# Performance work log

Measured on AMD Instinct MI355X. Metric: run time of the kernel, lower is better.

The kernel has to match this reference:

```python
import jax, jax.numpy as jnp
import numpy as np

B = 4096        # batch_size
D = 256         # feature_dim
N = 9000000     # dataset size (state buffer length)
G = 100         # num_groups
ALPHA = 0.5     # alpha_weight
GAMMA = 0.8
RHO = 8.0
LAM = 1.0       # lambada
ETA_P = 0.01
EPS = 1e-14
CLIP = 5.0


def setup_inputs() -> dict:
    key = jax.random.key(0)
    k = jax.random.split(key, 6)
    zis = jax.random.normal(k[0], (B, D), jnp.float32)
    zjs = jax.random.normal(k[1], (B, D), jnp.float32)
    # per-sample learned temperatures, small positive values
    taus_I = 0.01 + 0.2 * jax.random.uniform(k[2], (N,), jnp.float32)
    taus_T = 0.01 + 0.2 * jax.random.uniform(k[3], (N,), jnp.float32)
    group_info_I = jax.random.randint(k[4], (N,), 0, G, dtype=jnp.int32)
    group_info_T = jax.random.randint(k[5], (N,), 0, G, dtype=jnp.int32)
    ids = jnp.arange(B, dtype=jnp.int32)  # unique sample indices
    zeros_N = jnp.zeros((N,), jnp.float32)
    return {
        "zis": zis, "zjs": zjs,
        "s_I": zeros_N, "s_T": zeros_N, "b_I": zeros_N, "b_T": zeros_N,
        "z_I": jnp.zeros((G,), jnp.float32), "z_T": jnp.zeros((G,), jnp.float32),
        "p_I": jnp.ones((G,), jnp.float32) / G, "p_T": jnp.ones((G,), jnp.float32) / G,
        "taus_I": taus_I, "taus_T": taus_T,
        "ids": ids, "group_info_I": group_info_I, "group_info_T": group_info_T,
    }


def _l2norm(x):
    return x / jnp.maximum(jnp.linalg.norm(x, axis=1, keepdims=True), 1e-12)


def reference(zis, zjs, s_I, s_T, b_I, b_T, z_I, z_T, p_I, p_T,
              taus_I, taus_T, ids, group_info_I, group_info_T):
    zis = _l2norm(zis)
    zjs = _l2norm(zjs)
    sim = zis @ zjs.T                                   # [B, B]
    diag = jnp.diagonal(sim)                            # [B]
    mask_neg = 1.0 - jnp.eye(B, dtype=sim.dtype)
    image_diffs = sim - diag[:, None]
    text_diffs = sim - diag[None, :]

    tau_I = taus_I[ids]                                 # [B]
    tau_T = taus_T[ids]
    idt = jax.lax.stop_gradient(image_diffs / tau_I[:, None])
    tdt = jax.lax.stop_gradient(text_diffs / tau_T[None, :])

    # running max state (numerically-stable exp)
    old_b_I = b_I[ids]
    b_I_new = jnp.maximum(jnp.max(idt, axis=1), old_b_I)    # [B]
    old_b_T = b_T[ids]
    b_T_new = jnp.maximum(jnp.max(tdt, axis=0), old_b_T)    # [B]
    b_I = b_I.at[ids].set(b_I_new)
    b_T = b_T.at[ids].set(b_T_new)

    exp_I = jnp.exp(idt - b_I_new[:, None]) * mask_neg
    exp_T = jnp.exp(tdt - b_T_new[None, :]) * mask_neg
    g_I = jnp.sum(exp_I, axis=1)                         # [B]
    g_T = jnp.sum(exp_T, axis=0)                         # [B]

    # EMA of softmax denominators with max-rescaling
    s_I_new = (1.0 - GAMMA) * s_I[ids] * jnp.exp(old_b_I - b_I_new) + GAMMA * g_I
    s_T_new = (1.0 - GAMMA) * s_T[ids] * jnp.exp(old_b_T - b_T_new) + GAMMA * g_T
    s_I = s_I.at[ids].set(s_I_new)
    s_T = s_T.at[ids].set(s_T_new)
    s_I_c = jnp.maximum(s_I_new, EPS)
    s_T_c = jnp.maximum(s_T_new, EPS)

    w_I = exp_I / s_I_c[:, None]
    w_T = exp_T / s_T_c[None, :]

    gid_I = group_info_I[ids]                            # [B]
    gid_T = group_info_T[ids]
    gw_I = G * p_I[gid_I]                                # [B]
    gw_T = G * p_T[gid_T]

    image_loss = jnp.sum(w_I * gw_I[:, None] * image_diffs, axis=1)   # [B]
    text_loss = jnp.sum(w_T * gw_T[None, :] * text_diffs, axis=0)     # [B]
    total_loss = ALPHA * image_loss.mean() + (1.0 - ALPHA) * text_loss.mean()

    # per-group adversarial weight update
    F_I = tau_I * (jnp.log(s_I_c) + b_I_new + RHO)       # [B]
    F_T = tau_T * (jnp.log(s_T_c) + b_T_new + RHO)
    ones_b = jnp.ones((B,), sim.dtype)
    cnt_I = jnp.maximum(jax.ops.segment_sum(ones_b, gid_I, num_segments=G), 1.0)
    cnt_T = jnp.maximum(jax.ops.segment_sum(ones_b, gid_T, num_segments=G), 1.0)
    grad_p_I = jax.ops.segment_sum(F_I, gid_I, num_segments=G) / cnt_I
    grad_p_T = jax.ops.segment_sum(F_T, gid_T, num_segments=G) / cnt_T

    z_I = (1.0 - GAMMA) * z_I + GAMMA * grad_p_I
    z_T = (1.0 - GAMMA) * z_T + GAMMA * grad_p_T
    grad_hp_I = -LAM * jnp.log(p_I + EPS) - LAM
    grad_hp_T = -LAM * jnp.log(p_T + EPS) - LAM
    new_p_I = p_I * jnp.exp(2.0 * ETA_P * jnp.clip(z_I + grad_hp_I, -CLIP, CLIP))
    new_p_T = p_T * jnp.exp(2.0 * ETA_P * jnp.clip(z_T + grad_hp_T, -CLIP, CLIP))
    p_I = new_p_I / new_p_I.sum()
    p_T = new_p_T / new_p_T.sum()

    return total_loss, p_I, p_T
```

## Files before the change

### kernel.cpp

```cpp
#include <hip/hip_runtime.h>
#include <hip/hip_bf16.h>
#include <math.h>

#define BB 4096
#define DD 256
#define GG 100
#define GAMMA_C 0.8f
#define RHO_C 8.0f
#define ALPHA_C 0.5f
#define EPS_C 1e-14f
#define NSR 64
#define NSC 32

typedef __bf16 bf16x8 __attribute__((ext_vector_type(8)));
typedef float f32x16 __attribute__((ext_vector_type(16)));

__device__ inline int swzLoc(int r31, int k) {
    return ((k >> 4) << 9) | (((((k >> 3) & 1) << 5) | r31) << 3) | (k & 7);
}

__device__ inline float blockReduceSum(float v, float* lds) {
    for (int o = 32; o > 0; o >>= 1) v += __shfl_down(v, o);
    int lane = threadIdx.x & 63, wid = threadIdx.x >> 6;
    if (lane == 0) lds[wid] = v;
    __syncthreads();
    if (threadIdx.x == 0) {
        float r = lds[0];
        int nw = blockDim.x >> 6;
        for (int w = 1; w < nw; w++) r += lds[w];
        lds[0] = r;
    }
    __syncthreads();
    float r = lds[0];
    __syncthreads();
    return r;
}

__global__ void __launch_bounds__(256) norm_kernel(const float* __restrict__ zis,
                            const float* __restrict__ zjs,
                            ushort* __restrict__ zhi, ushort* __restrict__ zlo,
                            ushort* __restrict__ whi, ushort* __restrict__ wlo,
                            float* __restrict__ diag, float* __restrict__ acc) {
    __shared__ ushort st[4][8192];
    int rb = blockIdx.x;
    int wv = threadIdx.x >> 6, lane = threadIdx.x & 63;
    if (rb == 0) { acc[threadIdx.x] = 0.f; acc[threadIdx.x + 256] = 0.f; }
    for (int rr = 0; rr < 8; rr++) {
        int r = rb * 32 + wv * 8 + rr;
        float4 zv = *(const float4*)&zis[r * DD + lane * 4];
        float4 wv4 = *(const float4*)&zjs[r * DD + lane * 4];
        float sz = zv.x * zv.x + zv.y * zv.y + zv.z * zv.z + zv.w * zv.w;
        float sw = wv4.x * wv4.x + wv4.y * wv4.y + wv4.z * wv4.z + wv4.w * wv4.w;
        float dt = zv.x * wv4.x + zv.y * wv4.y + zv.z * wv4.z + zv.w * wv4.w;
        for (int mask = 1; mask <= 32; mask <<= 1) {
            sz += __shfl_xor(sz, mask);
            sw += __shfl_xor(sw, mask);
            dt += __shfl_xor(dt, mask);
        }
        float iz = 1.0f / fmaxf(sqrtf(sz), 1e-12f);
        float iw = 1.0f / fmaxf(sqrtf(sw), 1e-12f);
        if (lane == 0) diag[r] = dt * iz * iw;
        float nz[4] = {zv.x * iz, zv.y * iz, zv.z * iz, zv.w * iz};
        float nw[4] = {wv4.x * iw, wv4.y * iw, wv4.z * iw, wv4.w * iw};
        int r31 = wv * 8 + rr;
        for (int e = 0; e < 4; e++) {
            int k = lane * 4 + e;
            int li = swzLoc(r31, k);
            __hip_bfloat16 hz = __float2bfloat16(nz[e]);
            __hip_bfloat16 lz = __float2bfloat16(nz[e] - __bfloat162float(hz));
            __hip_bfloat16 hw = __float2bfloat16(nw[e]);
            __hip_bfloat16 lw = __float2bfloat16(nw[e] - __bfloat162float(hw));
            st[0][li] = *(ushort*)&hz;
            st[1][li] = *(ushort*)&lz;
            st[2][li] = *(ushort*)&hw;
            st[3][li] = *(ushort*)&lw;
        }
    }
    __syncthreads();
    size_t base = (size_t)rb * 8192;
    ushort* dsts[4] = {zhi + base, zlo + base, whi + base, wlo + base};
    for (int a = 0; a < 4; a++) {
        uint4* d = (uint4*)dsts[a];
        const uint4* s = (const uint4*)st[a];
        for (int it = 0; it < 4; it++) {
            int idx = it * 256 + threadIdx.x;
            d[idx] = s[idx];
        }
    }
}

__global__ void __launch_bounds__(256, 4) fused_tile(const ushort* __restrict__ Ahi,
        const ushort* __restrict__ Alo, const ushort* __restrict__ Bhi,
        const ushort* __restrict__ Blo, const float* __restrict__ diag,
        const float* __restrict__ tausI, const float* __restrict__ tausT,
        const int* __restrict__ ids,
        float* __restrict__ pmR, float* __restrict__ pgR, float* __restrict__ pwR,
        float* __restrict__ pmC, float* __restrict__ pgC, float* __restrict__ pwC) {
    __shared__ float rDiag[128], rITau[128];
    __shared__ float cDiag[64], cITau[64];
    __shared__ float cmS[4][64], cgS[4][64], cwS[4][64];

    int lane = threadIdx.x & 63;
    int wv = threadIdx.x >> 6;
    int bm = blockIdx.y * 128, bn = blockIdx.x * 64;
    int h = lane >> 5, cl = lane & 31;

    if (threadIdx.x < 128) {
        int r = bm + threadIdx.x;
        rDiag[threadIdx.x] = diag[r];
        rITau[threadIdx.x] = 1.0f / tausI[ids[r]];
    } else if (threadIdx.x < 192) {
        int c = bn + threadIdx.x - 128;
        cDiag[threadIdx.x - 128] = diag[c];
        cITau[threadIdx.x - 128] = 1.0f / tausT[ids[c]];
    }

    int aBase = (blockIdx.y * 4 + wv) * 8192;
    int b0 = (blockIdx.x * 2) * 8192;
    int b1 = b0 + 8192;
    int lofs = lane * 8;

    f32x16 acc[2] = {};
    bf16x8 ah, al, bh0, bl0, bh1, bl1;
    ah  = *(const bf16x8*)&Ahi[aBase + lofs];
    al  = *(const bf16x8*)&Alo[aBase + lofs];
    bh0 = *(const bf16x8*)&Bhi[b0 + lofs];
    bl0 = *(const bf16x8*)&Blo[b0 + lofs];
    bh1 = *(const bf16x8*)&Bhi[b1 + lofs];
    bl1 = *(const bf16x8*)&Blo[b1 + lofs];
#pragma unroll
    for (int s = 0; s < 16; s++) {
        bf16x8 nah, nal, nbh0, nbl0, nbh1, nbl1;
        if (s < 15) {
            int so = (s + 1) * 512 + lofs;
            nah  = *(const bf16x8*)&Ahi[aBase + so];
            nal  = *(const bf16x8*)&Alo[aBase + so];
            nbh0 = *(const bf16x8*)&Bhi[b0 + so];
            nbl0 = *(const bf16x8*)&Blo[b0 + so];
            nbh1 = *(const bf16x8*)&Bhi[b1 + so];
            nbl1 = *(const bf16x8*)&Blo[b1 + so];
        }
        acc[0] = __builtin_amdgcn_mfma_f32_32x32x16_bf16(ah, bh0, acc[0], 0, 0, 0);
        acc[0] = __builtin_amdgcn_mfma_f32_32x32x16_bf16(ah, bl0, acc[0], 0, 0, 0);
        acc[0] = __builtin_amdgcn_mfma_f32_32x32x16_bf16(al, bh0, acc[0], 0, 0, 0);
        acc[1] = __builtin_amdgcn_mfma_f32_32x32x16_bf16(ah, bh1, acc[1], 0, 0, 0);
        acc[1] = __builtin_amdgcn_mfma_f32_32x32x16_bf16(ah, bl1, acc[1], 0, 0, 0);
        acc[1] = __builtin_amdgcn_mfma_f32_32x32x16_bf16(al, bh1, acc[1], 0, 0, 0);
        ah = nah; al = nal; bh0 = nbh0; bl0 = nbl0; bh1 = nbh1; bl1 = nbl1;
    }
    __syncthreads();

    float cd2[2], cit2[2], cbloc[2], cg[2] = {}, cw[2] = {};
    for (int u = 0; u < 2; u++) {
        int clc = u * 32 + cl;
        cd2[u] = cDiag[clc];
        cit2[u] = cITau[clc];
        float m = -INFINITY;
        for (int reg = 0; reg < 16; reg++) m = fmaxf(m, acc[u][reg]);
        m = fmaxf(m, __shfl_xor(m, 32));
        cbloc[u] = (m - cd2[u]) * cit2[u];
    }
    for (int u = 0; u < 2; u++) {
        int gc = bn + u * 32 + cl;
        for (int reg = 0; reg < 16; reg++) {
            int gr = bm + wv * 32 + (reg & 3) + 4 * h + 8 * (reg >> 2);
            float v = acc[u][reg];
            bool off = gr != gc;
            float dvT = v - cd2[u];
            float eT = off ? __expf(dvT * cit2[u] - cbloc[u]) : 0.f;
            cg[u] += eT;
            cw[u] += eT * dvT;
        }
    }
    for (int u = 0; u < 2; u++) {
        cg[u] += __shfl_xor(cg[u], 32);
        cw[u] += __shfl_xor(cw[u], 32);
        if (h == 0) {
            cmS[wv][u * 32 + cl] = cbloc[u];
            cgS[wv][u * 32 + cl] = cg[u];
            cwS[wv][u * 32 + cl] = cw[u];
        }
    }
    __syncthreads();
    if (threadIdx.x < 64) {
        int c = threadIdx.x;
        float m = fmaxf(fmaxf(cmS[0][c], cmS[1][c]), fmaxf(cmS[2][c], cmS[3][c]));
        float g = 0.f, w = 0.f;
        for (int wq = 0; wq < 4; wq++) {
            float f = __expf(cmS[wq][c] - m);
            g += cgS[wq][c] * f;
            w += cwS[wq][c] * f;
        }
        size_t o = (size_t)blockIdx.y * BB + bn + c;
        pmC[o] = m;
        pgC[o] = g;
        pwC[o] = w;
    }

    int stripeR = blockIdx.x;
    for (int q = 0; q < 4; q++) {
        float rd4[4], rit4[4], bloc[4], rg[4] = {}, rw[4] = {};
        for (int j = 0; j < 4; j++) {
            int rl = wv * 32 + 8 * q + 4 * h + j;
            rd4[j] = rDiag[rl];
            rit4[j] = rITau[rl];
        }
        for (int j = 0; j < 4; j++) {
            float m = fmaxf(acc[0][4 * q + j], acc[1][4 * q + j]);
            for (int mask = 1; mask <= 16; mask <<= 1)
                m = fmaxf(m, __shfl_xor(m, mask));
            bloc[j] = (m - rd4[j]) * rit4[j];
        }
        for (int u = 0; u < 2; u++) {
            int gc = bn + u * 32 + cl;
            for (int j = 0; j < 4; j++) {
                int gr = bm + wv * 32 + 8 * q + 4 * h + j;
                float v = acc[u][4 * q + j];
                bool off = gr != gc;
                float dvI = v - rd4[j];
                float eI = off ? __expf(dvI * rit4[j] - bloc[j]) : 0.f;
                rg[j] += eI;
                rw[j] += eI * dvI;
            }
        }
        for (int j = 0; j < 4; j++)
            for (int mask = 1; mask <= 16; mask <<= 1) {
                rg[j] += __shfl_xor(rg[j], mask);
                rw[j] += __shfl_xor(rw[j], mask);
            }
        if (cl == 0) {
            size_t o = (size_t)stripeR * BB + bm + wv * 32 + 8 * q + 4 * h;
            *(float4*)&pmR[o] = make_float4(bloc[0], bloc[1], bloc[2], bloc[3]);
            *(float4*)&pgR[o] = make_float4(rg[0], rg[1], rg[2], rg[3]);
            *(float4*)&pwR[o] = make_float4(rw[0], rw[1], rw[2], rw[3]);
        }
    }
}

__global__ void __launch_bounds__(256) fin_kernel(
        const float* __restrict__ pmR, const float* __restrict__ pgR,
        const float* __restrict__ pwR, const float* __restrict__ pmC,
        const float* __restrict__ pgC, const float* __restrict__ pwC,
        const float* __restrict__ sI, const float* __restrict__ bI,
        const float* __restrict__ tausI, const int* __restrict__ gInfI,
        const float* __restrict__ pI,
        const float* __restrict__ sT, const float* __restrict__ bT,
        const float* __restrict__ tausT, const int* __restrict__ gInfT,
        const float* __restrict__ pT,
        const int* __restrict__ ids, float* __restrict__ acc,
        const float* __restrict__ zI, const float* __restrict__ zT,
        float* __restrict__ out) {
    __shared__ float lds[8];
    __shared__ float binF[GG], binC[GG];
    __shared__ float mS[4][64], gS[4][64], wS[4][64];
    __shared__ int lastFlag;
    if (threadIdx.x < GG) { binF[threadIdx.x] = 0.f; binC[threadIdx.x] = 0.f; }
    int side = blockIdx.x >> 6;
    int chunk = blockIdx.x & 63;
    int il = threadIdx.x & 63;
    int sg = threadIdx.x >> 6;
    int i = chunk * 64 + il;
    int ns = side ? NSC : NSR;
    const float* pm = side ? pmC : pmR;
    const float* pg = side ? pgC : pgR;
    const float* pw = side ? pwC : pwR;
    const float* sS = side ? sT : sI;
    const float* bS = side ? bT : bI;
    const float* taus = side ? tausT : tausI;
    const int* ginfo = side ? gInfT : gInfI;
    const float* pP = side ? pT : pI;

    float m = -INFINITY, g = 0.f, w = 0.f;
    for (int s = sg; s < ns; s += 4) {
        float pms = pm[(size_t)s * BB + i];
        float pgs = pg[(size_t)s * BB + i];
        float pws = pw[(size_t)s * BB + i];
        float mn = fmaxf(m, pms);
        float fo = __expf(m - mn);
        float fs = __expf(pms - mn);
        g = g * fo + pgs * fs;
        w = w * fo + pws * fs;
        m = mn;
    }
    mS[sg][il] = m;
    gS[sg][il] = g;
    wS[sg][il] = w;
    __syncthreads();

    float loss = 0.f;
    if (sg == 0) {
        int id = ids[i];
        float oldb = bS[id];
        float mm = fmaxf(fmaxf(mS[0][il], mS[1][il]), fmaxf(mS[2][il], mS[3][il]));
        float bfin = fmaxf(mm, oldb);
        float gg2 = 0.f, ww2 = 0.f;
        for (int q = 0; q < 4; q++) {
            float f = __expf(mS[q][il] - bfin);
            gg2 += gS[q][il] * f;
            ww2 += wS[q][il] * f;
        }
        float tau = taus[id];
        float snew = (1.f - GAMMA_C) * sS[id] * expf(oldb - bfin) + GAMMA_C * gg2;
        float sc = fmaxf(snew, EPS_C);
        int gid = ginfo[id];
        float gw = (float)GG * pP[gid];
        loss = gw * ww2 / sc;
        float F = tau * (logf(sc) + bfin + RHO_C);
        atomicAdd(&binF[gid], F);
        atomicAdd(&binC[gid], 1.0f);
    }
    float lsum = blockReduceSum(loss, lds);
    if (threadIdx.x == 0) atomicAdd(&acc[side], lsum);
    __syncthreads();
    if (threadIdx.x < GG) {
        atomicAdd(&acc[2 + side * 200 + threadIdx.x], binF[threadIdx.x]);
        atomicAdd(&acc[102 + side * 200 + threadIdx.x], binC[threadIdx.x]);
    }

    __threadfence();
    if (threadIdx.x == 0) {
        int old = atomicAdd((int*)&acc[408], 1);
        lastFlag = (old == 127);
    }
    __syncthreads();
    if (!lastFlag) return;

    int gg = threadIdx.x;
    float npI = 0.f, npT = 0.f;
    if (gg < GG) {
        float cI = __hip_atomic_load(&acc[102 + gg], __ATOMIC_RELAXED, __HIP_MEMORY_SCOPE_AGENT);
        float fI = __hip_atomic_load(&acc[2 + gg], __ATOMIC_RELAXED, __HIP_MEMORY_SCOPE_AGENT);
        float gpI = fI / fmaxf(cI, 1.f);
        float zi = (1.f - GAMMA_C) * zI[gg] + GAMMA_C * gpI;
        float ghpI = -logf(pI[gg] + EPS_C) - 1.f;
        float ti = fminf(fmaxf(zi + ghpI, -5.f), 5.f);
        npI = pI[gg] * expf(0.02f * ti);

        float cT = __hip_atomic_load(&acc[302 + gg], __ATOMIC_RELAXED, __HIP_MEMORY_SCOPE_AGENT);
        float fT = __hip_atomic_load(&acc[202 + gg], __ATOMIC_RELAXED, __HIP_MEMORY_SCOPE_AGENT);
        float gpT = fT / fmaxf(cT, 1.f);
        float zt = (1.f - GAMMA_C) * zT[gg] + GAMMA_C * gpT;
        float ghpT = -logf(pT[gg] + EPS_C) - 1.f;
        float tt = fminf(fmaxf(zt + ghpT, -5.f), 5.f);
        npT = pT[gg] * expf(0.02f * tt);
    }
    float sumI = blockReduceSum(npI, lds);
    float sumT = blockReduceSum(npT, lds);
    if (gg < GG) {
        out[1 + gg] = npI / sumI;
        out[101 + gg] = npT / sumT;
    }
    if (gg == 0) {
        float lI = __hip_atomic_load(&acc[0], __ATOMIC_RELAXED, __HIP_MEMORY_SCOPE_AGENT);
        float lT = __hip_atomic_load(&acc[1], __ATOMIC_RELAXED, __HIP_MEMORY_SCOPE_AGENT);
        out[0] = ALPHA_C * (lI / (float)BB) + (1.f - ALPHA_C) * (lT / (float)BB);
    }
}

extern "C" void kernel_launch(void* const* d_in, const int* in_sizes, int n_in,
                              void* d_out, int out_size, void* d_ws, size_t ws_size,
                              hipStream_t stream) {
    const float* zis   = (const float*)d_in[0];
    const float* zjs   = (const float*)d_in[1];
    const float* s_I   = (const float*)d_in[2];
    const float* s_T   = (const float*)d_in[3];
    const float* b_I   = (const float*)d_in[4];
    const float* b_T   = (const float*)d_in[5];
    const float* z_I   = (const float*)d_in[6];
    const float* z_T   = (const float*)d_in[7];
    const float* p_I   = (const float*)d_in[8];
    const float* p_T   = (const float*)d_in[9];
    const float* tausI = (const float*)d_in[10];
    const float* tausT = (const float*)d_in[11];
    const int*   ids   = (const int*)d_in[12];
    const int*   gInfI = (const int*)d_in[13];
    const int*   gInfT = (const int*)d_in[14];
    float* out = (float*)d_out;

    char* ws = (char*)d_ws;
    ushort* zhi = (ushort*)ws;
    ushort* zlo = zhi + (size_t)BB * DD;
    ushort* whi = zlo + (size_t)BB * DD;
    ushort* wlo = whi + (size_t)BB * DD;
    float* acc  = (float*)(wlo + (size_t)BB * DD);
    float* diag = acc + 512;
    float* pmR  = diag + BB;
    float* pgR  = pmR + (size_t)NSR * BB;
    float* pwR  = pgR + (size_t)NSR * BB;
    float* pmC  = pwR + (size_t)NSR * BB;
    float* pgC  = pmC + (size_t)NSC * BB;
    float* pwC  = pgC + (size_t)NSC * BB;

    norm_kernel<<<128, 256, 0, stream>>>(zis, zjs, zhi, zlo, whi, wlo, diag, acc);
    fused_tile<<<dim3(64, 32), 256, 0, stream>>>(zhi, zlo, whi, wlo, diag,
            tausI, tausT, ids, pmR, pgR, pwR, pmC, pgC, pwC);
    fin_kernel<<<128, 256, 0, stream>>>(pmR, pgR, pwR, pmC, pgC, pwC,
            s_I, b_I, tausI, gInfI, p_I, s_T, b_T, tausT, gInfT, p_T, ids, acc,
            z_I, z_T, out);
}
```

Baseline: 280.8 us.

## Compute transposed similarity tile with extra MFMAs to avoid row-reduction shuffles

New measurement: 286.2 us. About the same (+1.9%).

```diff
diff --git a/kernel.cpp b/kernel.cpp
--- a/kernel.cpp
+++ b/kernel.cpp
@@ -121,32 +121,28 @@
     int lofs = lane * 8;
 
     f32x16 acc[2] = {};
-    bf16x8 ah, al, bh0, bl0, bh1, bl1;
-    ah  = *(const bf16x8*)&Ahi[aBase + lofs];
-    al  = *(const bf16x8*)&Alo[aBase + lofs];
-    bh0 = *(const bf16x8*)&Bhi[b0 + lofs];
-    bl0 = *(const bf16x8*)&Blo[b0 + lofs];
-    bh1 = *(const bf16x8*)&Bhi[b1 + lofs];
-    bl1 = *(const bf16x8*)&Blo[b1 + lofs];
+    f32x16 accT[2] = {};
 #pragma unroll
     for (int s = 0; s < 16; s++) {
-        bf16x8 nah, nal, nbh0, nbl0, nbh1, nbl1;
-        if (s < 15) {
-            int so = (s + 1) * 512 + lofs;
-            nah  = *(const bf16x8*)&Ahi[aBase + so];
-            nal  = *(const bf16x8*)&Alo[aBase + so];
-            nbh0 = *(const bf16x8*)&Bhi[b0 + so];
-            nbl0 = *(const bf16x8*)&Blo[b0 + so];
-            nbh1 = *(const bf16x8*)&Bhi[b1 + so];
-            nbl1 = *(const bf16x8*)&Blo[b1 + so];
-        }
-        acc[0] = __builtin_amdgcn_mfma_f32_32x32x16_bf16(ah, bh0, acc[0], 0, 0, 0);
-        acc[0] = __builtin_amdgcn_mfma_f32_32x32x16_bf16(ah, bl0, acc[0], 0, 0, 0);
-        acc[0] = __builtin_amdgcn_mfma_f32_32x32x16_bf16(al, bh0, acc[0], 0, 0, 0);
-        acc[1] = __builtin_amdgcn_mfma_f32_32x32x16_bf16(ah, bh1, acc[1], 0, 0, 0);
-        acc[1] = __builtin_amdgcn_mfma_f32_32x32x16_bf16(ah, bl1, acc[1], 0, 0, 0);
-        acc[1] = __builtin_amdgcn_mfma_f32_32x32x16_bf16(al, bh1, acc[1], 0, 0, 0);
-        ah = nah; al = nal; bh0 = nbh0; bl0 = nbl0; bh1 = nbh1; bl1 = nbl1;
+        int so = s * 512 + lofs;
+        bf16x8 ah  = *(const bf16x8*)&Ahi[aBase + so];
+        bf16x8 al  = *(const bf16x8*)&Alo[aBase + so];
+        bf16x8 bh0 = *(const bf16x8*)&Bhi[b0 + so];
+        bf16x8 bl0 = *(const bf16x8*)&Blo[b0 + so];
+        bf16x8 bh1 = *(const bf16x8*)&Bhi[b1 + so];
+        bf16x8 bl1 = *(const bf16x8*)&Blo[b1 + so];
+        acc[0]  = __builtin_amdgcn_mfma_f32_32x32x16_bf16(ah, bh0, acc[0], 0, 0, 0);
+        accT[0] = __builtin_amdgcn_mfma_f32_32x32x16_bf16(bh0, ah, accT[0], 0, 0, 0);
+        acc[1]  = __builtin_amdgcn_mfma_f32_32x32x16_bf16(ah, bh1, acc[1], 0, 0, 0);
+        accT[1] = __builtin_amdgcn_mfma_f32_32x32x16_bf16(bh1, ah, accT[1], 0, 0, 0);
+        acc[0]  = __builtin_amdgcn_mfma_f32_32x32x16_bf16(ah, bl0, acc[0], 0, 0, 0);
+        accT[0] = __builtin_amdgcn_mfma_f32_32x32x16_bf16(bh0, al, accT[0], 0, 0, 0);
+        acc[1]  = __builtin_amdgcn_mfma_f32_32x32x16_bf16(ah, bl1, acc[1], 0, 0, 0);
+        accT[1] = __builtin_amdgcn_mfma_f32_32x32x16_bf16(bh1, al, accT[1], 0, 0, 0);
+        acc[0]  = __builtin_amdgcn_mfma_f32_32x32x16_bf16(al, bh0, acc[0], 0, 0, 0);
+        accT[0] = __builtin_amdgcn_mfma_f32_32x32x16_bf16(bl0, ah, accT[0], 0, 0, 0);
+        acc[1]  = __builtin_amdgcn_mfma_f32_32x32x16_bf16(al, bh1, acc[1], 0, 0, 0);
+        accT[1] = __builtin_amdgcn_mfma_f32_32x32x16_bf16(bl1, ah, accT[1], 0, 0, 0);
     }
     __syncthreads();
 
@@ -197,42 +193,35 @@
         pwC[o] = w;
     }
 
-    int stripeR = blockIdx.x;
-    for (int q = 0; q < 4; q++) {
-        float rd4[4], rit4[4], bloc[4], rg[4] = {}, rw[4] = {};
-        for (int j = 0; j < 4; j++) {
-            int rl = wv * 32 + 8 * q + 4 * h + j;
-            rd4[j] = rDiag[rl];
-            rit4[j] = rITau[rl];
-        }
-        for (int j = 0; j < 4; j++) {
-            float m = fmaxf(acc[0][4 * q + j], acc[1][4 * q + j]);
-            for (int mask = 1; mask <= 16; mask <<= 1)
-                m = fmaxf(m, __shfl_xor(m, mask));
-            bloc[j] = (m - rd4[j]) * rit4[j];
-        }
+    {
+        int gr = bm + wv * 32 + cl;
+        float rd = rDiag[wv * 32 + cl];
+        float rit = rITau[wv * 32 + cl];
+        float m = -INFINITY;
+        for (int u = 0; u < 2; u++)
+            for (int reg = 0; reg < 16; reg++)
+                m = fmaxf(m, accT[u][reg]);
+        m = fmaxf(m, __shfl_xor(m, 32));
+        float bloc = (m - rd) * rit;
+        float rg = 0.f, rw = 0.f;
         for (int u = 0; u < 2; u++) {
-            int gc = bn + u * 32 + cl;
-            for (int j = 0; j < 4; j++) {
-                int gr = bm + wv * 32 + 8 * q + 4 * h + j;
-                float v = acc[u][4 * q + j];
+            for (int reg = 0; reg < 16; reg++) {
+                int gc = bn + u * 32 + (reg & 3) + 4 * h + 8 * (reg >> 2);
+                float v = accT[u][reg];
                 bool off = gr != gc;
-                float dvI = v - rd4[j];
-                float eI = off ? __expf(dvI * rit4[j] - bloc[j]) : 0.f;
-                rg[j] += eI;
-                rw[j] += eI * dvI;
+                float dvI = v - rd;
+                float eI = off ? __expf(dvI * rit - bloc) : 0.f;
+                rg += eI;
+                rw += eI * dvI;
             }
         }
-        for (int j = 0; j < 4; j++)
-            for (int mask = 1; mask <= 16; mask <<= 1) {
-                rg[j] += __shfl_xor(rg[j], mask);
-                rw[j] += __shfl_xor(rw[j], mask);
-            }
-        if (cl == 0) {
-            size_t o = (size_t)stripeR * BB + bm + wv * 32 + 8 * q + 4 * h;
-            *(float4*)&pmR[o] = make_float4(bloc[0], bloc[1], bloc[2], bloc[3]);
-            *(float4*)&pgR[o] = make_float4(rg[0], rg[1], rg[2], rg[3]);
-            *(float4*)&pwR[o] = make_float4(rw[0], rw[1], rw[2], rw[3]);
+        rg += __shfl_xor(rg, 32);
+        rw += __shfl_xor(rw, 32);
+        if (h == 0) {
+            size_t o = (size_t)blockIdx.x * BB + bm + wv * 32 + cl;
+            pmR[o] = bloc;
+            pgR[o] = rg;
+            pwR[o] = rw;
         }
     }
 }
```
